# Kernel optimization log

Measured on AMD Instinct MI355X. Metric: run time of the kernel, lower is better.

The kernel has to match this reference:

```python
import jax, jax.numpy as jnp
from jax import lax
import numpy as np

EMA_ALPHA = 0.3
LN_EPS = 1e-5
SW = 5  # center_window_size


def _gelu(x):
    return jax.nn.gelu(x, approximate=False)  # torch nn.GELU default = exact erf


def _layernorm(x, g, b):
    mu = x.mean(-1, keepdims=True)
    var = ((x - mu) ** 2).mean(-1, keepdims=True)
    return (x - mu) * lax.rsqrt(var + LN_EPS) * g + b


def _ema_scan(x, alpha):
    # x: [B, T, C]; x_smooth[t] = lerp(x_smooth[t-1], x[t], alpha)
    x0 = x[:, 0]
    def step(prev, xt):
        s = prev + alpha * (xt - prev)
        return s, s
    _, ys = lax.scan(step, x0, jnp.swapaxes(x[:, 1:], 0, 1))  # [T-1, B, C]
    return jnp.concatenate([x0[:, None], jnp.swapaxes(ys, 0, 1)], axis=1)


def _lstm_dir(x, w_ih, w_hh, b):
    # x: [B, T, Cin]; w_ih: [Cin, 4H]; w_hh: [H, 4H]; b: [4H]. torch gate order i,f,g,o
    B = x.shape[0]
    H = w_hh.shape[0]
    pre = jnp.einsum('btc,ch->bth', x, w_ih) + b  # [B, T, 4H]
    def step(carry, p):
        h, c = carry
        gates = p + h @ w_hh
        i, f, g, o = jnp.split(gates, 4, axis=-1)
        c = jax.nn.sigmoid(f) * c + jax.nn.sigmoid(i) * jnp.tanh(g)
        h = jax.nn.sigmoid(o) * jnp.tanh(c)
        return (h, c), h
    init = (jnp.zeros((B, H), x.dtype), jnp.zeros((B, H), x.dtype))
    _, hs = lax.scan(step, init, jnp.swapaxes(pre, 0, 1))  # [T, B, H]
    return jnp.swapaxes(hs, 0, 1)


def _bilstm(x, wih_f, whh_f, b_f, wih_r, whh_r, b_r):
    fwd = _lstm_dir(x, wih_f, whh_f, b_f)
    bwd = jnp.flip(_lstm_dir(jnp.flip(x, axis=1), wih_r, whh_r, b_r), axis=1)
    return jnp.concatenate([fwd, bwd], axis=-1)  # [B, T, 2H]


def setup_inputs() -> dict:
    key = jax.random.key(0)
    ks = jax.random.split(key, 24)
    B, T, C, BD, O, H = 4096, 31, 768, 128, 12, 64
    AUG = 3 * BD  # 384
    def n(k, shape, s):
        return jax.random.normal(k, shape, dtype=jnp.float32) * s
    return {
        'x': n(ks[0], (B, T, C), 1.0),
        'cls_w': n(ks[1], (C, BD), 0.03), 'cls_b': jnp.zeros((BD,), jnp.float32),
        'delta_w': n(ks[2], (C, BD), 0.03), 'delta_b': jnp.zeros((BD,), jnp.float32),
        'acc_w': n(ks[3], (C, BD), 0.03), 'acc_b': jnp.zeros((BD,), jnp.float32),
        'cls_ln_g': jnp.ones((BD,), jnp.float32), 'cls_ln_b': jnp.zeros((BD,), jnp.float32),
        'delta_ln_g': jnp.ones((BD,), jnp.float32), 'delta_ln_b': jnp.zeros((BD,), jnp.float32),
        'acc_ln_g': jnp.ones((BD,), jnp.float32), 'acc_ln_b': jnp.zeros((BD,), jnp.float32),
        'lin0_w': n(ks[4], (AUG, 256), 0.05), 'lin0_b': jnp.zeros((256,), jnp.float32),
        'gate': jnp.float32(0.2),
        'attn_w': n(ks[5], (2 * H, 1), 0.08), 'attn_b': jnp.zeros((1,), jnp.float32),
        'attn_temp': jnp.float32(1.0),
        'lin1_w': n(ks[6], (C, O), 0.03), 'lin1_b': jnp.zeros((O,), jnp.float32),
        'lin2_w': n(ks[7], (2 * H, O), 0.08), 'lin2_b': jnp.zeros((O,), jnp.float32),
        'lstm_wih_f': n(ks[8], (256, 4 * H), 0.06), 'lstm_whh_f': n(ks[9], (H, 4 * H), 0.12),
        'lstm_b_f': jnp.zeros((4 * H,), jnp.float32),
        'lstm_wih_r': n(ks[10], (256, 4 * H), 0.06), 'lstm_whh_r': n(ks[11], (H, 4 * H), 0.12),
        'lstm_b_r': jnp.zeros((4 * H,), jnp.float32),
    }


def reference(x, cls_w, cls_b, delta_w, delta_b, acc_w, acc_b,
              cls_ln_g, cls_ln_b, delta_ln_g, delta_ln_b, acc_ln_g, acc_ln_b,
              lin0_w, lin0_b, gate, attn_w, attn_b, attn_temp,
              lin1_w, lin1_b, lin2_w, lin2_b,
              lstm_wih_f, lstm_whh_f, lstm_b_f, lstm_wih_r, lstm_whh_r, lstm_b_r):
    T = x.shape[1]
    hsl = T // 2
    l, r = max(0, hsl - SW), min(T, hsl + SW + 1)  # center window [10, 21) for T=31

    # --- robust deltas: EMA smoothing + reflect-padded finite differences ---
    x_smooth = _ema_scan(x, EMA_ALPHA)                       # [B, T, C]
    padded = jnp.pad(x_smooth, ((0, 0), (2, 0), (0, 0)), mode='reflect')  # [B, T+2, C]
    dx = padded[:, 1:] - padded[:, :-1]                       # [B, T+1, C]
    ddx = dx[:, 1:] - dx[:, :-1]                              # [B, T, C]
    delta_stream = dx[:, 1:]                                  # [B, T, C]
    acc_stream = ddx                                          # [B, T, C]

    # --- linear branch: mean of lin1 over center window of smoothed stream ---
    linear_logits = (x_smooth[:, l:r] @ lin1_w + lin1_b).mean(axis=1)  # [B, O]

    # --- bottlenecks (eval mode: dropout identity) + LayerNorms ---
    cls_bn = _layernorm(_gelu(x_smooth @ cls_w + cls_b), cls_ln_g, cls_ln_b)
    delta_bn = _layernorm(_gelu(delta_stream @ delta_w + delta_b), delta_ln_g, delta_ln_b)
    acc_bn = _layernorm(_gelu(acc_stream @ acc_w + acc_b), acc_ln_g, acc_ln_b)
    x_aug = jnp.concatenate([cls_bn, delta_bn, acc_bn], axis=-1)  # [B, T, 384]

    x_lstm = _gelu(x_aug @ lin0_w + lin0_b)                   # [B, T, 256]
    x_lstm = x_lstm - x_lstm.mean(axis=1, keepdims=True)      # center over time (fp32)

    # --- BiLSTM + attention pooling over center window ---
    lstm_out = _bilstm(x_lstm, lstm_wih_f, lstm_whh_f, lstm_b_f,
                       lstm_wih_r, lstm_whh_r, lstm_b_r)      # [B, T, 128]
    window = lstm_out[:, l:r]                                 # [B, W, 128]
    temp = jax.nn.softplus(attn_temp) + 0.001
    scores = (window @ attn_w + attn_b)[..., 0] / temp        # [B, W]
    attn = jax.nn.softmax(scores, axis=1)[..., None]          # [B, W, 1]
    attended = (attn * window).sum(axis=1)                    # [B, 128]
    lstm_logits = attended @ lin2_w + lin2_b                  # [B, O]

    g = jax.nn.sigmoid(gate)
    final_logits = linear_logits + g * (lstm_logits - linear_logits)
    return final_logits, attended
```

## Files before the change

### kernel.cpp

```cpp
#include <hip/hip_runtime.h>
#include <cstdint>
#include <cstddef>


typedef short s8v __attribute__((ext_vector_type(8)));
typedef float f4v __attribute__((ext_vector_type(4)));

#if defined(__has_builtin)
#if __has_builtin(__builtin_amdgcn_global_load_lds)
#define HAVE_GLL 1
#endif
#endif
#ifndef HAVE_GLL
#define HAVE_GLL 0
#endif

__device__ __forceinline__ unsigned short f2bf(float f) {
  union { float f; unsigned int u; } v; v.f = f;
  unsigned int u = v.u;
  return (unsigned short)((u + 0x7fffu + ((u >> 16) & 1u)) >> 16);
}
__device__ __forceinline__ float bf2f(unsigned short h) {
  union { unsigned int u; float f; } v; v.u = ((unsigned int)h) << 16;
  return v.f;
}
__device__ __forceinline__ float fsig(float x) {
  return __fdividef(1.f, 1.f + __expf(-x));
}
__device__ __forceinline__ float ftanh(float x) {
  return 1.f - __fdividef(2.f, 1.f + __expf(2.f * x));
}
__device__ __forceinline__ float fgelu(float x) {
  return 0.5f * x * (1.f + erff(x * 0.70710678118654752f));
}

__device__ __forceinline__ void ld_lds16(const unsigned short* g,
                                         unsigned short* ldsU, int lane) {
#if HAVE_GLL
  __builtin_amdgcn_global_load_lds(
      (__attribute__((address_space(1))) void*)(uintptr_t)(const void*)g,
      (__attribute__((address_space(3))) void*)(unsigned int)(uintptr_t)(void*)ldsU,
      16, 0, 0);
#else
  *(uint4*)(ldsU + lane * 8) = *(const uint4*)g;
#endif
}
__device__ __forceinline__ void wait_vm0() {
#if HAVE_GLL
  __builtin_amdgcn_s_waitcnt(0x0F70);
#endif
}

#define OFF_W1T   0u
#define OFF_W2T   589824u
#define OFF_WIHT  786432u
#define OFF_WHHT  1048576u
#define OFF_XS    1114112u
#define OFF_XW    196149248u
#define OFF_LL    208732160u
#define OFF_WIN   208928768u
#define OFF_XAUG  220463104u
#define OFF_XLSTM 317980672u

__global__ __launch_bounds__(256) void k0_prep(
    const float* __restrict__ cls_w, const float* __restrict__ delta_w,
    const float* __restrict__ acc_w, const float* __restrict__ lin0_w,
    const float* __restrict__ wih_f, const float* __restrict__ wih_r,
    const float* __restrict__ whh_f, const float* __restrict__ whh_r,
    unsigned short* __restrict__ ws) {
  int i = blockIdx.x * 256 + threadIdx.x;
  if (i < 294912) {
    int n = i / 768, k = i - n * 768;
    int seg = n >> 7, nn = n & 127;
    const float* w = seg == 0 ? cls_w : (seg == 1 ? delta_w : acc_w);
    ws[i] = f2bf(w[k * 128 + nn]);
  } else if (i < 393216) {
    int j = i - 294912;
    int n = j / 384, k = j - n * 384;
    ws[i] = f2bf(lin0_w[k * 256 + n]);
  } else if (i < 524288) {
    int j = i - 393216;
    int n = j >> 8, k = j & 255;
    ws[i] = f2bf(n < 256 ? wih_f[k * 256 + n] : wih_r[k * 256 + (n - 256)]);
  } else if (i < 557056) {
    int j = i - 524288;
    int d = j >> 14, rem = j & 16383;
    int n = rem >> 6, k = rem & 63;
    const float* w = d ? whh_r : whh_f;
    ws[i] = f2bf(w[k * 256 + n]);
  }
}

__global__ __launch_bounds__(256) void k1_ema(
    const float* __restrict__ x, unsigned short* __restrict__ xs,
    float* __restrict__ xw) {
  int gid = blockIdx.x * 256 + threadIdx.x;
  int b = gid / 768;
  int c = gid - b * 768;
  size_t base = (size_t)b * 31 * 768 + c;
  float s = x[base];
  xs[base] = f2bf(s);
  float wsum = 0.f;
#pragma unroll
  for (int t = 1; t < 31; ++t) {
    float xv = x[base + t * 768];
    s = s + 0.3f * (xv - s);
    xs[base + t * 768] = f2bf(s);
    if (t >= 10 && t <= 20) wsum += s;
  }
  xw[gid] = wsum * (1.f / 11.f);
}

__global__ __launch_bounds__(64) void k1b_linlog(
    const float* __restrict__ xw, const float* __restrict__ lin1_w,
    const float* __restrict__ lin1_b, float* __restrict__ ll) {
  int b = blockIdx.x;
  int lane = threadIdx.x;
  float p[12];
#pragma unroll
  for (int o = 0; o < 12; ++o) p[o] = 0.f;
  for (int k = lane; k < 768; k += 64) {
    float xv = xw[b * 768 + k];
    const float* w = lin1_w + k * 12;
#pragma unroll
    for (int o = 0; o < 12; ++o) p[o] += xv * w[o];
  }
#pragma unroll
  for (int o = 0; o < 12; ++o) {
    float v = p[o];
#pragma unroll
    for (int s = 1; s < 64; s <<= 1) v += __shfl_xor(v, s, 64);
    p[o] = v;
  }
  if (lane == 0) {
#pragma unroll
    for (int o = 0; o < 12; ++o) ll[b * 12 + o] = p[o] + lin1_b[o];
  }
}

template <int KDIM>
__device__ __forceinline__ void gemm128(
    const unsigned short* __restrict__ A, int rowClamp,
    const unsigned short* __restrict__ Bt,
    unsigned short* sA, unsigned short* sB, f4v acc[4][4]) {
  const int tid  = threadIdx.x;
  const int lane = tid & 63;
  const int wv   = tid >> 6;
  const int l15  = lane & 15;
  const int quad = lane >> 4;
  const int mh   = (wv >> 1) * 64;
  const int nh   = (wv & 1) * 64;

  const int srow = wv * 32 + (lane >> 3);
  const int scol = (lane & 7) * 8;
  const unsigned short* aBase[4];
  const unsigned short* bBase[4];
  unsigned short* aDst[4];
  unsigned short* bDst[4];
#pragma unroll
  for (int j = 0; j < 4; ++j) {
    int r = srow + j * 8;
    int ar = r < rowClamp ? r : rowClamp;
    aBase[j] = A + (size_t)ar * KDIM + scol;
    bBase[j] = Bt + (size_t)r * KDIM + scol;
    aDst[j] = sA + (wv * 4 + j) * 512;
    bDst[j] = sB + (wv * 4 + j) * 512;
  }
#pragma unroll
  for (int mt = 0; mt < 4; ++mt)
#pragma unroll
    for (int nt = 0; nt < 4; ++nt)
      acc[mt][nt] = (f4v){0.f, 0.f, 0.f, 0.f};

  constexpr int KT = KDIM / 64;
  for (int kt = 0; kt < KT; ++kt) {
    if (kt) __syncthreads();
    int ko = kt * 64;
#pragma unroll
    for (int j = 0; j < 4; ++j) ld_lds16(aBase[j] + ko, aDst[j], lane);
#pragma unroll
    for (int j = 0; j < 4; ++j) ld_lds16(bBase[j] + ko, bDst[j], lane);
    wait_vm0();
    __syncthreads();
#pragma unroll
    for (int ks = 0; ks < 2; ++ks) {
      s8v af[4], bfv[4];
#pragma unroll
      for (int mt = 0; mt < 4; ++mt)
        af[mt] = *(const s8v*)(&sA[(mh + mt * 16 + l15) * 64 + ks * 32 + quad * 8]);
#pragma unroll
      for (int nt = 0; nt < 4; ++nt)
        bfv[nt] = *(const s8v*)(&sB[(nh + nt * 16 + l15) * 64 + ks * 32 + quad * 8]);
#pragma unroll
      for (int mt = 0; mt < 4; ++mt)
#pragma unroll
        for (int nt = 0; nt < 4; ++nt)
          acc[mt][nt] = __builtin_amdgcn_mfma_f32_16x16x32_bf16(af[mt], bfv[nt], acc[mt][nt], 0, 0, 0);
    }
  }
  __syncthreads();
}

__device__ __forceinline__ void dump_chunk(f4v acc[4][4], float* sP, int lo,
                                           int nrows, int pstr) {
  const int tid  = threadIdx.x;
  const int lane = tid & 63;
  const int wv   = tid >> 6;
  const int l15  = lane & 15;
  const int quad = lane >> 4;
  const int mh   = (wv >> 1) * 64;
  const int nh   = (wv & 1) * 64;
#pragma unroll
  for (int mt = 0; mt < 4; ++mt)
#pragma unroll
    for (int nt = 0; nt < 4; ++nt)
#pragma unroll
      for (int r = 0; r < 4; ++r) {
        int rr = mh + mt * 16 + quad * 4 + r - lo;
        if ((unsigned)rr < (unsigned)nrows)
          sP[rr * pstr + nh + nt * 16 + l15] = acc[mt][nt][r];
      }
}

__device__ __forceinline__ float stencil_gelu3(const float* sP, const float* sBias,
                                               int seg, int t, int c) {
  const float* p = sP + t * 390 + seg * 130 + c;
  float v;
  if (seg == 0) {
    v = p[0];
  } else if (seg == 1) {
    v = (t == 0) ? (p[0] - p[390]) : (p[0] - p[-390]);
  } else {
    if (t == 0)      v = p[0] - 2.f * p[390] + p[780];
    else if (t == 1) v = 2.f * (p[0] - p[-390]);
    else             v = p[0] - 2.f * p[-390] + p[-780];
  }
  return fgelu(v + sBias[seg * 128 + c]);
}

__global__ __launch_bounds__(1024) void k2_aug(
    const unsigned short* __restrict__ xs, const unsigned short* __restrict__ W1t,
    const float* __restrict__ cls_b, const float* __restrict__ delta_b,
    const float* __restrict__ acc_b,
    const float* __restrict__ g0, const float* __restrict__ be0,
    const float* __restrict__ g1, const float* __restrict__ be1,
    const float* __restrict__ g2, const float* __restrict__ be2,
    unsigned short* __restrict__ xaug) {
  __shared__ __align__(16) char smem[131072];
  unsigned short* buf0 = (unsigned short*)smem;
  unsigned short* buf1 = (unsigned short*)(smem + 65536);
  float* sP    = (float*)smem;
  float* sBias = (float*)(smem + 65536);
  float* sG    = sBias + 384;
  float* sLb   = sG + 384;
  float* sMu   = sLb + 384;
  float* sRs   = sMu + 93;

  const int tid  = threadIdx.x;
  const int lane = tid & 63;
  const int wv   = tid >> 6;
  const int l15  = lane & 15;
  const int quad = lane >> 4;
  const int wm   = wv >> 3;
  const int wn   = wv & 7;
  const int rowBase = blockIdx.x * 124;

  const int subrow = lane >> 3;
  const int schunk = ((lane & 7) ^ subrow) * 8;
  const unsigned short* src[4];
#pragma unroll
  for (int j = 0; j < 4; ++j) {
    int slice = wv * 4 + j;
    int row = slice * 8 + subrow;
    src[j] = (row < 128)
        ? xs + (size_t)(rowBase + (row < 124 ? row : 123)) * 768 + schunk
        : W1t + (size_t)(row - 128) * 768 + schunk;
  }

  f4v acc[4][3];
#pragma unroll
  for (int mt = 0; mt < 4; ++mt)
#pragma unroll
    for (int nt = 0; nt < 3; ++nt) acc[mt][nt] = (f4v){0.f, 0.f, 0.f, 0.f};

  const int swz = (l15 & 7) << 3;

#pragma unroll
  for (int j = 0; j < 4; ++j) ld_lds16(src[j], buf0 + (wv * 4 + j) * 512, lane);
  wait_vm0();
  __syncthreads();

  for (int kt = 0; kt < 12; ++kt) {
    unsigned short* bc = (kt & 1) ? buf1 : buf0;
    unsigned short* bn = (kt & 1) ? buf0 : buf1;
    if (kt < 11) {
#pragma unroll
      for (int j = 0; j < 4; ++j)
        ld_lds16(src[j] + (kt + 1) * 64, bn + (wv * 4 + j) * 512, lane);
    }
#pragma unroll
    for (int ks = 0; ks < 2; ++ks) {
      s8v af[4], bfv[3];
      const int ko = (ks * 32 + quad * 8) ^ swz;
#pragma unroll
      for (int mt = 0; mt < 4; ++mt)
        af[mt] = *(const s8v*)(&bc[(wm * 64 + mt * 16 + l15) * 64 + ko]);
#pragma unroll
      for (int nt = 0; nt < 3; ++nt)
        bfv[nt] = *(const s8v*)(&bc[(128 + wn * 48 + nt * 16 + l15) * 64 + ko]);
#pragma unroll
      for (int mt = 0; mt < 4; ++mt)
#pragma unroll
        for (int nt = 0; nt < 3; ++nt)
          acc[mt][nt] = __builtin_amdgcn_mfma_f32_16x16x32_bf16(af[mt], bfv[nt], acc[mt][nt], 0, 0, 0);
    }
    wait_vm0();
    __syncthreads();
  }

  if (tid < 384) {
    int seg = tid >> 7, c = tid & 127;
    sBias[tid] = seg == 0 ? cls_b[c] : (seg == 1 ? delta_b[c] : acc_b[c]);
    sG[tid]    = seg == 0 ? g0[c]    : (seg == 1 ? g1[c]    : g2[c]);
    sLb[tid]   = seg == 0 ? be0[c]   : (seg == 1 ? be1[c]   : be2[c]);
  }

#pragma unroll
  for (int ck = 0; ck < 4; ++ck) {
    int lo = ck * 31;
#pragma unroll
    for (int mt = 0; mt < 4; ++mt) {
      int rbase = wm * 64 + mt * 16 + quad * 4 - lo;
#pragma unroll
      for (int nt = 0; nt < 3; ++nt) {
        int gcol = wn * 48 + nt * 16;
        int colp = (gcol >> 7) * 130 + (gcol & 127) + l15;
#pragma unroll
        for (int r = 0; r < 4; ++r) {
          int rr = rbase + r;
          if ((unsigned)rr < 31u) sP[rr * 390 + colp] = acc[mt][nt][r];
        }
      }
    }
    __syncthreads();
    if (tid < 744) {
      int seg = tid < 248 ? 0 : (tid < 496 ? 1 : 2);
      int rem = tid - seg * 248;
      int row = rem >> 3, q = rem & 7;
      float sum = 0.f, ss = 0.f;
#pragma unroll
      for (int i = 0; i < 16; ++i) {
        float v = stencil_gelu3(sP, sBias, seg, row, q + 8 * i);
        sum += v; ss += v * v;
      }
      sum += __shfl_xor(sum, 1, 64); ss += __shfl_xor(ss, 1, 64);
      sum += __shfl_xor(sum, 2, 64); ss += __shfl_xor(ss, 2, 64);
      sum += __shfl_xor(sum, 4, 64); ss += __shfl_xor(ss, 4, 64);
      if (q == 0) {
        float mu = sum * (1.f / 128.f);
        sMu[seg * 31 + row] = mu;
        sRs[seg * 31 + row] = rsqrtf(ss * (1.f / 128.f) - mu * mu + 1e-5f);
      }
    }
    __syncthreads();
#pragma unroll
    for (int seg = 0; seg < 3; ++seg) {
      for (int idx = tid; idx < 31 * 128; idx += 1024) {
        int row = idx >> 7, c = idx & 127;
        float v = stencil_gelu3(sP, sBias, seg, row, c);
        float o = (v - sMu[seg * 31 + row]) * sRs[seg * 31 + row]
                  * sG[seg * 128 + c] + sLb[seg * 128 + c];
        xaug[(size_t)(rowBase + lo + row) * 384 + seg * 128 + c] = f2bf(o);
      }
    }
    __syncthreads();
  }
}

__global__ __launch_bounds__(256) void k3_lstm_in(
    const unsigned short* __restrict__ xaug, const unsigned short* __restrict__ W2t,
    const float* __restrict__ lin0_b, unsigned short* __restrict__ xlstm) {
  __shared__ __align__(16) char smem[33792];
  unsigned short* sA = (unsigned short*)smem;
  unsigned short* sB = (unsigned short*)(smem + 16384);
  float* sP  = (float*)smem;
  float* sCM = (float*)(smem + 32768);
  int by = blockIdx.y;
  int rowBase = blockIdx.x * 124;
  f4v acc[4][4];
  gemm128<384>(xaug + (size_t)rowBase * 384, 123, W2t + (size_t)by * 128 * 384, sA, sB, acc);
  int tid = threadIdx.x;
#pragma unroll
  for (int ck = 0; ck < 2; ++ck) {
    int lo = ck * 62;
    dump_chunk(acc, sP, lo, 62, 132);
    __syncthreads();
    for (int idx = tid; idx < 62 * 128; idx += 256) {
      int row = idx >> 7, col = idx & 127;
      sP[row * 132 + col] = fgelu(sP[row * 132 + col] + lin0_b[by * 128 + col]);
    }
    __syncthreads();
    {
      int bb = tid >> 7, col = tid & 127;
      float s = 0.f;
      for (int tr = 0; tr < 31; ++tr) s += sP[(bb * 31 + tr) * 132 + col];
      sCM[tid] = s * (1.f / 31.f);
    }
    __syncthreads();
    for (int idx = tid; idx < 62 * 128; idx += 256) {
      int row = idx >> 7, col = idx & 127;
      int bb = row >= 31 ? 1 : 0;
      float v = sP[row * 132 + col] - sCM[bb * 128 + col];
      xlstm[(size_t)(rowBase + lo + row) * 256 + by * 128 + col] = f2bf(v);
    }
    __syncthreads();
  }
}

__global__ __launch_bounds__(256) void k3b_pre(
    const unsigned short* __restrict__ xlstm, const unsigned short* __restrict__ Wiht,
    const float* __restrict__ b_f, const float* __restrict__ b_r,
    unsigned short* __restrict__ pre) {
  __shared__ __align__(16) char smem[32768];
  unsigned short* sA = (unsigned short*)smem;
  unsigned short* sB = (unsigned short*)(smem + 16384);
  float* sP = (float*)smem;
  int by = blockIdx.y;
  int rowBase = blockIdx.x * 128;
  f4v acc[4][4];
  gemm128<256>(xlstm + (size_t)rowBase * 256, 127, Wiht + (size_t)by * 128 * 256, sA, sB, acc);
  int tid = threadIdx.x;
#pragma unroll
  for (int ck = 0; ck < 2; ++ck) {
    int lo = ck * 64;
    dump_chunk(acc, sP, lo, 64, 128);
    __syncthreads();
    for (int idx = tid; idx < 64 * 128; idx += 256) {
      int row = idx >> 7, col = idx & 127;
      int gcol = by * 128 + col;
      float bias = gcol < 256 ? b_f[gcol] : b_r[gcol - 256];
      pre[(size_t)(rowBase + lo + row) * 512 + gcol] = f2bf(sP[row * 128 + col] + bias);
    }
    __syncthreads();
  }
}

__global__ __launch_bounds__(256) void k4_lstm(
    const unsigned short* __restrict__ pre, const unsigned short* __restrict__ Whht,
    unsigned short* __restrict__ win) {
  __shared__ unsigned short sW[256 * 72];
  __shared__ unsigned short sH[16 * 72];
  __shared__ float sG[16 * 260];
  int tid = threadIdx.x;
  int dir = blockIdx.y;
  int b0  = blockIdx.x * 16;
  {
    const unsigned short* src = Whht + dir * 16384;
#pragma unroll
    for (int c = 0; c < 8; ++c) {
      int id = tid + c * 256;
      int row = id >> 3, kc = (id & 7) * 8;
      uint4 v = *(const uint4*)(src + row * 64 + kc);
      *(uint4*)(&sW[row * 72 + kc]) = v;
    }
  }
  for (int i = tid; i < 16 * 72; i += 256) sH[i] = 0;
  __syncthreads();

  const int lane = tid & 63, wv = tid >> 6, l15 = lane & 15, quad = lane >> 4;
  const int eb = tid >> 4, jb = (tid & 15) * 4;
  float cs[4] = {0.f, 0.f, 0.f, 0.f};

  int tt0 = dir ? 30 : 0;
  const unsigned short* pbase = pre + ((size_t)(b0 + eb) * 31) * 512 + dir * 256;
  ushort4 pi = *(const ushort4*)(pbase + tt0 * 512 + jb);
  ushort4 pf = *(const ushort4*)(pbase + tt0 * 512 + 64 + jb);
  ushort4 pg = *(const ushort4*)(pbase + tt0 * 512 + 128 + jb);
  ushort4 po = *(const ushort4*)(pbase + tt0 * 512 + 192 + jb);

  for (int t = 0; t < 31; ++t) {
    f4v acc[4];
#pragma unroll
    for (int nt = 0; nt < 4; ++nt) acc[nt] = (f4v){0.f, 0.f, 0.f, 0.f};
#pragma unroll
    for (int ks = 0; ks < 2; ++ks) {
      s8v af = *(const s8v*)(&sH[l15 * 72 + ks * 32 + quad * 8]);
#pragma unroll
      for (int nt = 0; nt < 4; ++nt) {
        int n = wv * 64 + nt * 16 + l15;
        s8v bfv = *(const s8v*)(&sW[n * 72 + ks * 32 + quad * 8]);
        acc[nt] = __builtin_amdgcn_mfma_f32_16x16x32_bf16(af, bfv, acc[nt], 0, 0, 0);
      }
    }
#pragma unroll
    for (int nt = 0; nt < 4; ++nt)
#pragma unroll
      for (int r = 0; r < 4; ++r)
        sG[(quad * 4 + r) * 260 + wv * 64 + nt * 16 + l15] = acc[nt][r];

    ushort4 ni, nf, ng, no;
    if (t < 30) {
      int ttn = dir ? 29 - t : t + 1;
      ni = *(const ushort4*)(pbase + ttn * 512 + jb);
      nf = *(const ushort4*)(pbase + ttn * 512 + 64 + jb);
      ng = *(const ushort4*)(pbase + ttn * 512 + 128 + jb);
      no = *(const ushort4*)(pbase + ttn * 512 + 192 + jb);
    }
    __syncthreads();

    int tt = dir ? 30 - t : t;
    const float* g = &sG[eb * 260];
    float hv[4];
#pragma unroll
    for (int jj = 0; jj < 4; ++jj) {
      int j = jb + jj;
      float vi = g[j]       + bf2f(jj == 0 ? pi.x : jj == 1 ? pi.y : jj == 2 ? pi.z : pi.w);
      float vf = g[64 + j]  + bf2f(jj == 0 ? pf.x : jj == 1 ? pf.y : jj == 2 ? pf.z : pf.w);
      float vg = g[128 + j] + bf2f(jj == 0 ? pg.x : jj == 1 ? pg.y : jj == 2 ? pg.z : pg.w);
      float vo = g[192 + j] + bf2f(jj == 0 ? po.x : jj == 1 ? po.y : jj == 2 ? po.z : po.w);
      float cc = fsig(vf) * cs[jj] + fsig(vi) * ftanh(vg);
      cs[jj] = cc;
      hv[jj] = fsig(vo) * ftanh(cc);
    }
    ushort4 hb;
    hb.x = f2bf(hv[0]); hb.y = f2bf(hv[1]); hb.z = f2bf(hv[2]); hb.w = f2bf(hv[3]);
    *(ushort4*)(&sH[eb * 72 + jb]) = hb;
    if (tt >= 10 && tt <= 20)
      *(ushort4*)(win + ((size_t)(b0 + eb) * 11 + (tt - 10)) * 128 + dir * 64 + jb) = hb;
    if (t < 30) { pi = ni; pf = nf; pg = ng; po = no; }
    __syncthreads();
  }
}

__global__ __launch_bounds__(256) void k5_attn(
    const unsigned short* __restrict__ win, const float* __restrict__ attn_w,
    const float* __restrict__ attn_b, const float* __restrict__ attn_t,
    const float* __restrict__ lin2_w, const float* __restrict__ lin2_b,
    const float* __restrict__ linlog, const float* __restrict__ gate,
    float* __restrict__ out) {
  __shared__ unsigned short sWin[176 * 128];
  __shared__ float sAw[128];
  __shared__ float sSc[176];
  __shared__ float sAtt[16 * 128];
  int tid = threadIdx.x;
  int b0  = blockIdx.x * 16;
#pragma unroll
  for (int c = 0; c < 11; ++c) {
    int id = tid + c * 256;
    int row = id >> 4, kc = (id & 15) * 8;
    uint4 v = *(const uint4*)(win + ((size_t)b0 * 11 + row) * 128 + kc);
    *(uint4*)(&sWin[row * 128 + kc]) = v;
  }
  if (tid < 128) sAw[tid] = attn_w[tid];
  __syncthreads();
  if (tid < 176) {
    int b = tid / 11, wt = tid - b * 11;
    const unsigned short* w = &sWin[(b * 11 + wt) * 128];
    float dot = 0.f;
    for (int ch = 0; ch < 128; ++ch) dot += bf2f(w[ch]) * sAw[ch];
    float temp = logf(1.f + __expf(attn_t[0])) + 0.001f;
    sSc[tid] = (dot + attn_b[0]) / temp;
  }
  __syncthreads();
  if (tid < 16) {
    float m = -1e30f;
    for (int wt = 0; wt < 11; ++wt) m = fmaxf(m, sSc[tid * 11 + wt]);
    float e[11], sum = 0.f;
    for (int wt = 0; wt < 11; ++wt) { e[wt] = __expf(sSc[tid * 11 + wt] - m); sum += e[wt]; }
    float inv = __fdividef(1.f, sum);
    for (int wt = 0; wt < 11; ++wt) sSc[tid * 11 + wt] = e[wt] * inv;
  }
  __syncthreads();
#pragma unroll
  for (int p = 0; p < 8; ++p) {
    int task = tid + p * 256;
    int b = task >> 7, ch = task & 127;
    float a = 0.f;
    for (int wt = 0; wt < 11; ++wt)
      a += sSc[b * 11 + wt] * bf2f(sWin[(b * 11 + wt) * 128 + ch]);
    sAtt[b * 128 + ch] = a;
    out[49152 + (size_t)(b0 + b) * 128 + ch] = a;
  }
  __syncthreads();
  if (tid < 192) {
    int b = tid / 12, o = tid - b * 12;
    float dot = 0.f;
    for (int ch = 0; ch < 128; ++ch) dot += sAtt[b * 128 + ch] * lin2_w[ch * 12 + o];
    dot += lin2_b[o];
    float lin = linlog[(size_t)(b0 + b) * 12 + o];
    float gg = fsig(gate[0]);
    out[(size_t)(b0 + b) * 12 + o] = lin + gg * (dot - lin);
  }
}

extern "C" void kernel_launch(void* const* d_in, const int* in_sizes, int n_in,
                              void* d_out, int out_size, void* d_ws, size_t ws_size,
                              hipStream_t stream) {
  const float* x       = (const float*)d_in[0];
  const float* cls_w   = (const float*)d_in[1];
  const float* cls_b   = (const float*)d_in[2];
  const float* delta_w = (const float*)d_in[3];
  const float* delta_b = (const float*)d_in[4];
  const float* acc_w   = (const float*)d_in[5];
  const float* acc_b   = (const float*)d_in[6];
  const float* cls_g   = (const float*)d_in[7];
  const float* cls_be  = (const float*)d_in[8];
  const float* del_g   = (const float*)d_in[9];
  const float* del_be  = (const float*)d_in[10];
  const float* accg    = (const float*)d_in[11];
  const float* accbe   = (const float*)d_in[12];
  const float* lin0_w  = (const float*)d_in[13];
  const float* lin0_b  = (const float*)d_in[14];
  const float* gate    = (const float*)d_in[15];
  const float* attn_w  = (const float*)d_in[16];
  const float* attn_b  = (const float*)d_in[17];
  const float* attn_t  = (const float*)d_in[18];
  const float* lin1_w  = (const float*)d_in[19];
  const float* lin1_b  = (const float*)d_in[20];
  const float* lin2_w  = (const float*)d_in[21];
  const float* lin2_b  = (const float*)d_in[22];
  const float* wih_f   = (const float*)d_in[23];
  const float* whh_f   = (const float*)d_in[24];
  const float* b_f     = (const float*)d_in[25];
  const float* wih_r   = (const float*)d_in[26];
  const float* whh_r   = (const float*)d_in[27];
  const float* b_r     = (const float*)d_in[28];

  char* ws = (char*)d_ws;
  unsigned short* W1t   = (unsigned short*)(ws + OFF_W1T);
  unsigned short* W2t   = (unsigned short*)(ws + OFF_W2T);
  unsigned short* Wiht  = (unsigned short*)(ws + OFF_WIHT);
  unsigned short* Whht  = (unsigned short*)(ws + OFF_WHHT);
  unsigned short* XS    = (unsigned short*)(ws + OFF_XS);
  unsigned short* PRE   = XS;
  float*          XW    = (float*)(ws + OFF_XW);
  float*          LL    = (float*)(ws + OFF_LL);
  unsigned short* WIN   = (unsigned short*)(ws + OFF_WIN);
  unsigned short* XAUG  = (unsigned short*)(ws + OFF_XAUG);
  unsigned short* XLSTM = (unsigned short*)(ws + OFF_XLSTM);
  float* out = (float*)d_out;

  k0_prep<<<2176, 256, 0, stream>>>(cls_w, delta_w, acc_w, lin0_w, wih_f, wih_r,
                                    whh_f, whh_r, (unsigned short*)ws);
  k1_ema<<<12288, 256, 0, stream>>>(x, XS, XW);
  k1b_linlog<<<4096, 64, 0, stream>>>(XW, lin1_w, lin1_b, LL);
  k2_aug<<<1024, 1024, 0, stream>>>(XS, W1t, cls_b, delta_b, acc_b,
                                    cls_g, cls_be, del_g, del_be, accg, accbe, XAUG);
  k3_lstm_in<<<dim3(1024, 2), 256, 0, stream>>>(XAUG, W2t, lin0_b, XLSTM);
  k3b_pre<<<dim3(992, 4), 256, 0, stream>>>(XLSTM, Wiht, b_f, b_r, PRE);
  k4_lstm<<<dim3(256, 2), 256, 0, stream>>>(PRE, Whht, WIN);
  k5_attn<<<256, 256, 0, stream>>>(WIN, attn_w, attn_b, attn_t, lin2_w, lin2_b,
                                   LL, gate, out);
}
```

Before: 1.101 ms.

## Fuse augment, LSTM-input and gate-preactivation GEMMs into one kernel

Merges k2_aug, k3_lstm_in and k3b_pre into a single 512-thread kernel that keeps the 124-row x_aug and x_lstm tiles in LDS. Weight tiles are streamed through double-buffered staging, and only the final gate preactivations go to global memory. This removes the global round trips for the bf16 XAUG and XLSTM intermediates and two kernel launches. In exchange it uses about 152 KB of LDS per block, so each CU holds fewer blocks and there is less latency hiding. The bias, centering and layernorm epilogues are also reorganised with wider per-thread work.

```diff
diff --git a/kernel.cpp b/kernel.cpp
--- a/kernel.cpp
+++ b/kernel.cpp
@@ -59,8 +59,7 @@
 #define OFF_XW    196149248u
 #define OFF_LL    208732160u
 #define OFF_WIN   208928768u
-#define OFF_XAUG  220463104u
-#define OFF_XLSTM 317980672u
+#define OFF_PRE   220463104u
 
 __global__ __launch_bounds__(256) void k0_prep(
     const float* __restrict__ cls_w, const float* __restrict__ delta_w,
@@ -138,185 +137,58 @@
   }
 }
 
-template <int KDIM>
-__device__ __forceinline__ void gemm128(
-    const unsigned short* __restrict__ A, int rowClamp,
-    const unsigned short* __restrict__ Bt,
-    unsigned short* sA, unsigned short* sB, f4v acc[4][4]) {
+__device__ __forceinline__ float stencil_gelu3(const float* sP, const float* sBias,
+                                               int seg, int t, int c) {
+  const float* p = sP + t * 388 + seg * 130 + c;
+  float v;
+  if (seg == 0) {
+    v = p[0];
+  } else if (seg == 1) {
+    v = (t == 0) ? (p[0] - p[388]) : (p[0] - p[-388]);
+  } else {
+    if (t == 0)      v = p[0] - 2.f * p[388] + p[776];
+    else if (t == 1) v = 2.f * (p[0] - p[-388]);
+    else             v = p[0] - 2.f * p[-388] + p[-776];
+  }
+  return fgelu(v + sBias[seg * 128 + c]);
+}
+
+__global__ __launch_bounds__(512, 2) void k2_mega(
+    const unsigned short* __restrict__ xs, const unsigned short* __restrict__ W1t,
+    const unsigned short* __restrict__ W2t, const unsigned short* __restrict__ Wiht,
+    const float* __restrict__ cls_b, const float* __restrict__ delta_b,
+    const float* __restrict__ acc_b,
+    const float* __restrict__ g0, const float* __restrict__ be0,
+    const float* __restrict__ g1, const float* __restrict__ be1,
+    const float* __restrict__ g2, const float* __restrict__ be2,
+    const float* __restrict__ lin0_b, const float* __restrict__ b_f,
+    const float* __restrict__ b_r, unsigned short* __restrict__ pre) {
+  __shared__ __align__(16) char smem[156160];
+  unsigned short* stg1  = (unsigned short*)smem;
+  unsigned short* xaug  = (unsigned short*)smem;
+  unsigned short* xlstm = (unsigned short*)smem;
+  unsigned short* stg3  = (unsigned short*)(smem + 65536);
+  unsigned short* sPb   = (unsigned short*)(smem + 65536);
+  float*          sP1   = (float*)(smem + 98304);
+  unsigned short* stg2  = (unsigned short*)(smem + 98304);
+  float*          sP2   = (float*)(smem + 98304);
+  float* sBias = (float*)(smem + 146688);
+  float* sG    = sBias + 384;
+  float* sLb   = sG + 384;
+  float* sMu   = sLb + 384;
+  float* sRs   = sMu + 93;
+  float* sL0b  = sRs + 93;
+  float* sB3   = sL0b + 256;
+  float* sCM   = sB3 + 512;
+
   const int tid  = threadIdx.x;
   const int lane = tid & 63;
   const int wv   = tid >> 6;
   const int l15  = lane & 15;
   const int quad = lane >> 4;
-  const int mh   = (wv >> 1) * 64;
-  const int nh   = (wv & 1) * 64;
-
-  const int srow = wv * 32 + (lane >> 3);
-  const int scol = (lane & 7) * 8;
-  const unsigned short* aBase[4];
-  const unsigned short* bBase[4];
-  unsigned short* aDst[4];
-  unsigned short* bDst[4];
-#pragma unroll
-  for (int j = 0; j < 4; ++j) {
-    int r = srow + j * 8;
-    int ar = r < rowClamp ? r : rowClamp;
-    aBase[j] = A + (size_t)ar * KDIM + scol;
-    bBase[j] = Bt + (size_t)r * KDIM + scol;
-    aDst[j] = sA + (wv * 4 + j) * 512;
-    bDst[j] = sB + (wv * 4 + j) * 512;
-  }
-#pragma unroll
-  for (int mt = 0; mt < 4; ++mt)
-#pragma unroll
-    for (int nt = 0; nt < 4; ++nt)
-      acc[mt][nt] = (f4v){0.f, 0.f, 0.f, 0.f};
-
-  constexpr int KT = KDIM / 64;
-  for (int kt = 0; kt < KT; ++kt) {
-    if (kt) __syncthreads();
-    int ko = kt * 64;
-#pragma unroll
-    for (int j = 0; j < 4; ++j) ld_lds16(aBase[j] + ko, aDst[j], lane);
-#pragma unroll
-    for (int j = 0; j < 4; ++j) ld_lds16(bBase[j] + ko, bDst[j], lane);
-    wait_vm0();
-    __syncthreads();
-#pragma unroll
-    for (int ks = 0; ks < 2; ++ks) {
-      s8v af[4], bfv[4];
-#pragma unroll
-      for (int mt = 0; mt < 4; ++mt)
-        af[mt] = *(const s8v*)(&sA[(mh + mt * 16 + l15) * 64 + ks * 32 + quad * 8]);
-#pragma unroll
-      for (int nt = 0; nt < 4; ++nt)
-        bfv[nt] = *(const s8v*)(&sB[(nh + nt * 16 + l15) * 64 + ks * 32 + quad * 8]);
-#pragma unroll
-      for (int mt = 0; mt < 4; ++mt)
-#pragma unroll
-        for (int nt = 0; nt < 4; ++nt)
-          acc[mt][nt] = __builtin_amdgcn_mfma_f32_16x16x32_bf16(af[mt], bfv[nt], acc[mt][nt], 0, 0, 0);
-    }
-  }
-  __syncthreads();
-}
-
-__device__ __forceinline__ void dump_chunk(f4v acc[4][4], float* sP, int lo,
-                                           int nrows, int pstr) {
-  const int tid  = threadIdx.x;
-  const int lane = tid & 63;
-  const int wv   = tid >> 6;
-  const int l15  = lane & 15;
-  const int quad = lane >> 4;
-  const int mh   = (wv >> 1) * 64;
-  const int nh   = (wv & 1) * 64;
-#pragma unroll
-  for (int mt = 0; mt < 4; ++mt)
-#pragma unroll
-    for (int nt = 0; nt < 4; ++nt)
-#pragma unroll
-      for (int r = 0; r < 4; ++r) {
-        int rr = mh + mt * 16 + quad * 4 + r - lo;
-        if ((unsigned)rr < (unsigned)nrows)
-          sP[rr * pstr + nh + nt * 16 + l15] = acc[mt][nt][r];
-      }
-}
-
-__device__ __forceinline__ float stencil_gelu3(const float* sP, const float* sBias,
-                                               int seg, int t, int c) {
-  const float* p = sP + t * 390 + seg * 130 + c;
-  float v;
-  if (seg == 0) {
-    v = p[0];
-  } else if (seg == 1) {
-    v = (t == 0) ? (p[0] - p[390]) : (p[0] - p[-390]);
-  } else {
-    if (t == 0)      v = p[0] - 2.f * p[390] + p[780];
-    else if (t == 1) v = 2.f * (p[0] - p[-390]);
-    else             v = p[0] - 2.f * p[-390] + p[-780];
-  }
-  return fgelu(v + sBias[seg * 128 + c]);
-}
-
-__global__ __launch_bounds__(1024) void k2_aug(
-    const unsigned short* __restrict__ xs, const unsigned short* __restrict__ W1t,
-    const float* __restrict__ cls_b, const float* __restrict__ delta_b,
-    const float* __restrict__ acc_b,
-    const float* __restrict__ g0, const float* __restrict__ be0,
-    const float* __restrict__ g1, const float* __restrict__ be1,
-    const float* __restrict__ g2, const float* __restrict__ be2,
-    unsigned short* __restrict__ xaug) {
-  __shared__ __align__(16) char smem[131072];
-  unsigned short* buf0 = (unsigned short*)smem;
-  unsigned short* buf1 = (unsigned short*)(smem + 65536);
-  float* sP    = (float*)smem;
-  float* sBias = (float*)(smem + 65536);
-  float* sG    = sBias + 384;
-  float* sLb   = sG + 384;
-  float* sMu   = sLb + 384;
-  float* sRs   = sMu + 93;
-
-  const int tid  = threadIdx.x;
-  const int lane = tid & 63;
-  const int wv   = tid >> 6;
-  const int l15  = lane & 15;
-  const int quad = lane >> 4;
-  const int wm   = wv >> 3;
-  const int wn   = wv & 7;
+  const int wm   = wv >> 2;
+  const int wn   = wv & 3;
   const int rowBase = blockIdx.x * 124;
-
-  const int subrow = lane >> 3;
-  const int schunk = ((lane & 7) ^ subrow) * 8;
-  const unsigned short* src[4];
-#pragma unroll
-  for (int j = 0; j < 4; ++j) {
-    int slice = wv * 4 + j;
-    int row = slice * 8 + subrow;
-    src[j] = (row < 128)
-        ? xs + (size_t)(rowBase + (row < 124 ? row : 123)) * 768 + schunk
-        : W1t + (size_t)(row - 128) * 768 + schunk;
-  }
-
-  f4v acc[4][3];
-#pragma unroll
-  for (int mt = 0; mt < 4; ++mt)
-#pragma unroll
-    for (int nt = 0; nt < 3; ++nt) acc[mt][nt] = (f4v){0.f, 0.f, 0.f, 0.f};
-
-  const int swz = (l15 & 7) << 3;
-
-#pragma unroll
-  for (int j = 0; j < 4; ++j) ld_lds16(src[j], buf0 + (wv * 4 + j) * 512, lane);
-  wait_vm0();
-  __syncthreads();
-
-  for (int kt = 0; kt < 12; ++kt) {
-    unsigned short* bc = (kt & 1) ? buf1 : buf0;
-    unsigned short* bn = (kt & 1) ? buf0 : buf1;
-    if (kt < 11) {
-#pragma unroll
-      for (int j = 0; j < 4; ++j)
-        ld_lds16(src[j] + (kt + 1) * 64, bn + (wv * 4 + j) * 512, lane);
-    }
-#pragma unroll
-    for (int ks = 0; ks < 2; ++ks) {
-      s8v af[4], bfv[3];
-      const int ko = (ks * 32 + quad * 8) ^ swz;
-#pragma unroll
-      for (int mt = 0; mt < 4; ++mt)
-        af[mt] = *(const s8v*)(&bc[(wm * 64 + mt * 16 + l15) * 64 + ko]);
-#pragma unroll
-      for (int nt = 0; nt < 3; ++nt)
-        bfv[nt] = *(const s8v*)(&bc[(128 + wn * 48 + nt * 16 + l15) * 64 + ko]);
-#pragma unroll
-      for (int mt = 0; mt < 4; ++mt)
-#pragma unroll
-        for (int nt = 0; nt < 3; ++nt)
-          acc[mt][nt] = __builtin_amdgcn_mfma_f32_16x16x32_bf16(af[mt], bfv[nt], acc[mt][nt], 0, 0, 0);
-    }
-    wait_vm0();
-    __syncthreads();
-  }
 
   if (tid < 384) {
     int seg = tid >> 7, c = tid & 127;
@@ -324,38 +196,89 @@
     sG[tid]    = seg == 0 ? g0[c]    : (seg == 1 ? g1[c]    : g2[c]);
     sLb[tid]   = seg == 0 ? be0[c]   : (seg == 1 ? be1[c]   : be2[c]);
   }
-
-#pragma unroll
+  if (tid < 256) sL0b[tid] = lin0_b[tid];
+  sB3[tid] = tid < 256 ? b_f[tid] : b_r[tid - 256];
+
+  const int subrow  = lane >> 3;
+  const int schunk8 = ((lane & 7) ^ subrow) * 8;
+  const int swz     = (l15 & 7) << 3;
+  const unsigned short* src1[8];
+#pragma unroll
+  for (int j = 0; j < 8; ++j) {
+    int row = (wv * 8 + j) * 8 + subrow;
+    src1[j] = (row < 128)
+        ? xs + (size_t)(rowBase + (row < 124 ? row : 123)) * 768 + schunk8
+        : W1t + (size_t)(row - 128) * 768 + schunk8;
+  }
+
+  f4v acc1[4][6];
+#pragma unroll
+  for (int mt = 0; mt < 4; ++mt)
+#pragma unroll
+    for (int nt = 0; nt < 6; ++nt) acc1[mt][nt] = (f4v){0.f, 0.f, 0.f, 0.f};
+
+#pragma unroll
+  for (int j = 0; j < 8; ++j) ld_lds16(src1[j], stg1 + (wv * 8 + j) * 512, lane);
+  wait_vm0();
+  __syncthreads();
+
+  for (int kt = 0; kt < 12; ++kt) {
+    unsigned short* bc = stg1 + (kt & 1) * 32768;
+    unsigned short* bn = stg1 + ((kt & 1) ^ 1) * 32768;
+    if (kt < 11) {
+#pragma unroll
+      for (int j = 0; j < 8; ++j)
+        ld_lds16(src1[j] + (kt + 1) * 64, bn + (wv * 8 + j) * 512, lane);
+    }
+#pragma unroll
+    for (int ks = 0; ks < 2; ++ks) {
+      const int ko = (ks * 32 + quad * 8) ^ swz;
+      s8v af[4], bfv[6];
+#pragma unroll
+      for (int mt = 0; mt < 4; ++mt)
+        af[mt] = *(const s8v*)(&bc[(wm * 64 + mt * 16 + l15) * 64 + ko]);
+#pragma unroll
+      for (int nt = 0; nt < 6; ++nt)
+        bfv[nt] = *(const s8v*)(&bc[(128 + wn * 96 + nt * 16 + l15) * 64 + ko]);
+#pragma unroll
+      for (int mt = 0; mt < 4; ++mt)
+#pragma unroll
+        for (int nt = 0; nt < 6; ++nt)
+          acc1[mt][nt] = __builtin_amdgcn_mfma_f32_16x16x32_bf16(af[mt], bfv[nt], acc1[mt][nt], 0, 0, 0);
+    }
+    wait_vm0();
+    __syncthreads();
+  }
+
   for (int ck = 0; ck < 4; ++ck) {
-    int lo = ck * 31;
+    const int lo = ck * 31;
 #pragma unroll
     for (int mt = 0; mt < 4; ++mt) {
       int rbase = wm * 64 + mt * 16 + quad * 4 - lo;
 #pragma unroll
-      for (int nt = 0; nt < 3; ++nt) {
-        int gcol = wn * 48 + nt * 16;
+      for (int nt = 0; nt < 6; ++nt) {
+        int gcol = wn * 96 + nt * 16;
         int colp = (gcol >> 7) * 130 + (gcol & 127) + l15;
 #pragma unroll
         for (int r = 0; r < 4; ++r) {
           int rr = rbase + r;
-          if ((unsigned)rr < 31u) sP[rr * 390 + colp] = acc[mt][nt][r];
+          if ((unsigned)rr < 31u) sP1[rr * 388 + colp] = acc1[mt][nt][r];
         }
       }
     }
     __syncthreads();
-    if (tid < 744) {
-      int seg = tid < 248 ? 0 : (tid < 496 ? 1 : 2);
-      int rem = tid - seg * 248;
-      int row = rem >> 3, q = rem & 7;
+    if (tid < 372) {
+      int seg = tid < 124 ? 0 : (tid < 248 ? 1 : 2);
+      int rem = tid - seg * 124;
+      int row = rem >> 2, q = rem & 3;
       float sum = 0.f, ss = 0.f;
 #pragma unroll
-      for (int i = 0; i < 16; ++i) {
-        float v = stencil_gelu3(sP, sBias, seg, row, q + 8 * i);
+      for (int i = 0; i < 32; ++i) {
+        float v = stencil_gelu3(sP1, sBias, seg, row, q + 4 * i);
         sum += v; ss += v * v;
       }
       sum += __shfl_xor(sum, 1, 64); ss += __shfl_xor(ss, 1, 64);
       sum += __shfl_xor(sum, 2, 64); ss += __shfl_xor(ss, 2, 64);
-      sum += __shfl_xor(sum, 4, 64); ss += __shfl_xor(ss, 4, 64);
       if (q == 0) {
         float mu = sum * (1.f / 128.f);
         sMu[seg * 31 + row] = mu;
@@ -365,83 +288,164 @@
     __syncthreads();
 #pragma unroll
     for (int seg = 0; seg < 3; ++seg) {
-      for (int idx = tid; idx < 31 * 128; idx += 1024) {
-        int row = idx >> 7, c = idx & 127;
-        float v = stencil_gelu3(sP, sBias, seg, row, c);
-        float o = (v - sMu[seg * 31 + row]) * sRs[seg * 31 + row]
-                  * sG[seg * 128 + c] + sLb[seg * 128 + c];
-        xaug[(size_t)(rowBase + lo + row) * 384 + seg * 128 + c] = f2bf(o);
-      }
-    }
-    __syncthreads();
-  }
-}
-
-__global__ __launch_bounds__(256) void k3_lstm_in(
-    const unsigned short* __restrict__ xaug, const unsigned short* __restrict__ W2t,
-    const float* __restrict__ lin0_b, unsigned short* __restrict__ xlstm) {
-  __shared__ __align__(16) char smem[33792];
-  unsigned short* sA = (unsigned short*)smem;
-  unsigned short* sB = (unsigned short*)(smem + 16384);
-  float* sP  = (float*)smem;
-  float* sCM = (float*)(smem + 32768);
-  int by = blockIdx.y;
-  int rowBase = blockIdx.x * 124;
-  f4v acc[4][4];
-  gemm128<384>(xaug + (size_t)rowBase * 384, 123, W2t + (size_t)by * 128 * 384, sA, sB, acc);
-  int tid = threadIdx.x;
-#pragma unroll
-  for (int ck = 0; ck < 2; ++ck) {
-    int lo = ck * 62;
-    dump_chunk(acc, sP, lo, 62, 132);
-    __syncthreads();
-    for (int idx = tid; idx < 62 * 128; idx += 256) {
-      int row = idx >> 7, col = idx & 127;
-      sP[row * 132 + col] = fgelu(sP[row * 132 + col] + lin0_b[by * 128 + col]);
-    }
-    __syncthreads();
-    {
-      int bb = tid >> 7, col = tid & 127;
+      for (int idx = tid; idx < 31 * 64; idx += 512) {
+        int row = idx >> 6, cp = (idx & 63) * 2;
+        float v0 = stencil_gelu3(sP1, sBias, seg, row, cp);
+        float v1 = stencil_gelu3(sP1, sBias, seg, row, cp + 1);
+        float mu = sMu[seg * 31 + row], rs = sRs[seg * 31 + row];
+        float o0 = (v0 - mu) * rs * sG[seg * 128 + cp]     + sLb[seg * 128 + cp];
+        float o1 = (v1 - mu) * rs * sG[seg * 128 + cp + 1] + sLb[seg * 128 + cp + 1];
+        unsigned int u = (unsigned int)f2bf(o0) | ((unsigned int)f2bf(o1) << 16);
+        *(unsigned int*)(&xaug[(size_t)(lo + row) * 392 + seg * 128 + cp]) = u;
+      }
+    }
+    __syncthreads();
+  }
+
+  f4v acc2[4][4];
+#pragma unroll
+  for (int mt = 0; mt < 4; ++mt)
+#pragma unroll
+    for (int nt = 0; nt < 4; ++nt) acc2[mt][nt] = (f4v){0.f, 0.f, 0.f, 0.f};
+  {
+    const int r2 = lane >> 2;
+    const int c2 = ((lane & 3) ^ (r2 & 3)) * 8;
+    const unsigned short* src2[2];
+#pragma unroll
+    for (int j = 0; j < 2; ++j)
+      src2[j] = W2t + (size_t)((wv * 2 + j) * 16 + r2) * 384 + c2;
+#pragma unroll
+    for (int j = 0; j < 2; ++j) ld_lds16(src2[j], stg2 + (wv * 2 + j) * 512, lane);
+    wait_vm0();
+    __syncthreads();
+    const int bko = (quad ^ (l15 & 3)) << 3;
+    for (int kt = 0; kt < 12; ++kt) {
+      unsigned short* bc = stg2 + (kt & 1) * 8192;
+      unsigned short* bn = stg2 + ((kt & 1) ^ 1) * 8192;
+      if (kt < 11) {
+#pragma unroll
+        for (int j = 0; j < 2; ++j)
+          ld_lds16(src2[j] + (kt + 1) * 32, bn + (wv * 2 + j) * 512, lane);
+      }
+      s8v af[4], bfv[4];
+#pragma unroll
+      for (int mt = 0; mt < 4; ++mt)
+        af[mt] = *(const s8v*)(&xaug[(size_t)(wm * 64 + mt * 16 + l15) * 392 + kt * 32 + quad * 8]);
+#pragma unroll
+      for (int nt = 0; nt < 4; ++nt)
+        bfv[nt] = *(const s8v*)(&bc[(wn * 64 + nt * 16 + l15) * 32 + bko]);
+#pragma unroll
+      for (int mt = 0; mt < 4; ++mt)
+#pragma unroll
+        for (int nt = 0; nt < 4; ++nt)
+          acc2[mt][nt] = __builtin_amdgcn_mfma_f32_16x16x32_bf16(af[mt], bfv[nt], acc2[mt][nt], 0, 0, 0);
+      wait_vm0();
+      __syncthreads();
+    }
+  }
+
+  for (int ck = 0; ck < 4; ++ck) {
+    const int lo = ck * 31;
+#pragma unroll
+    for (int mt = 0; mt < 4; ++mt) {
+      int rbase = wm * 64 + mt * 16 + quad * 4 - lo;
+#pragma unroll
+      for (int nt = 0; nt < 4; ++nt) {
+        int col = wn * 64 + nt * 16 + l15;
+#pragma unroll
+        for (int r = 0; r < 4; ++r) {
+          int rr = rbase + r;
+          if ((unsigned)rr < 31u) sP2[rr * 260 + col] = acc2[mt][nt][r];
+        }
+      }
+    }
+    __syncthreads();
+    for (int idx = tid; idx < 31 * 256; idx += 512) {
+      int row = idx >> 8, col = idx & 255;
+      sP2[row * 260 + col] = fgelu(sP2[row * 260 + col] + sL0b[col]);
+    }
+    __syncthreads();
+    if (tid < 256) {
       float s = 0.f;
-      for (int tr = 0; tr < 31; ++tr) s += sP[(bb * 31 + tr) * 132 + col];
+      for (int tr = 0; tr < 31; ++tr) s += sP2[tr * 260 + tid];
       sCM[tid] = s * (1.f / 31.f);
     }
     __syncthreads();
-    for (int idx = tid; idx < 62 * 128; idx += 256) {
-      int row = idx >> 7, col = idx & 127;
-      int bb = row >= 31 ? 1 : 0;
-      float v = sP[row * 132 + col] - sCM[bb * 128 + col];
-      xlstm[(size_t)(rowBase + lo + row) * 256 + by * 128 + col] = f2bf(v);
-    }
-    __syncthreads();
-  }
-}
-
-__global__ __launch_bounds__(256) void k3b_pre(
-    const unsigned short* __restrict__ xlstm, const unsigned short* __restrict__ Wiht,
-    const float* __restrict__ b_f, const float* __restrict__ b_r,
-    unsigned short* __restrict__ pre) {
-  __shared__ __align__(16) char smem[32768];
-  unsigned short* sA = (unsigned short*)smem;
-  unsigned short* sB = (unsigned short*)(smem + 16384);
-  float* sP = (float*)smem;
-  int by = blockIdx.y;
-  int rowBase = blockIdx.x * 128;
-  f4v acc[4][4];
-  gemm128<256>(xlstm + (size_t)rowBase * 256, 127, Wiht + (size_t)by * 128 * 256, sA, sB, acc);
-  int tid = threadIdx.x;
-#pragma unroll
-  for (int ck = 0; ck < 2; ++ck) {
-    int lo = ck * 64;
-    dump_chunk(acc, sP, lo, 64, 128);
-    __syncthreads();
-    for (int idx = tid; idx < 64 * 128; idx += 256) {
-      int row = idx >> 7, col = idx & 127;
-      int gcol = by * 128 + col;
-      float bias = gcol < 256 ? b_f[gcol] : b_r[gcol - 256];
-      pre[(size_t)(rowBase + lo + row) * 512 + gcol] = f2bf(sP[row * 128 + col] + bias);
-    }
-    __syncthreads();
+    for (int idx = tid; idx < 31 * 128; idx += 512) {
+      int row = idx >> 7, cp = (idx & 127) * 2;
+      float v0 = sP2[row * 260 + cp]     - sCM[cp];
+      float v1 = sP2[row * 260 + cp + 1] - sCM[cp + 1];
+      unsigned int u = (unsigned int)f2bf(v0) | ((unsigned int)f2bf(v1) << 16);
+      *(unsigned int*)(&xlstm[(size_t)(lo + row) * 260 + cp]) = u;
+    }
+    __syncthreads();
+  }
+
+  f4v acc3[4][4];
+  for (int p = 0; p < 2; ++p) {
+    const unsigned short* src3[4];
+#pragma unroll
+    for (int j = 0; j < 4; ++j)
+      src3[j] = Wiht + (size_t)(p * 256 + (wv * 4 + j) * 8 + subrow) * 256 + schunk8;
+#pragma unroll
+    for (int mt = 0; mt < 4; ++mt)
+#pragma unroll
+      for (int nt = 0; nt < 4; ++nt) acc3[mt][nt] = (f4v){0.f, 0.f, 0.f, 0.f};
+#pragma unroll
+    for (int j = 0; j < 4; ++j) ld_lds16(src3[j], stg3 + (wv * 4 + j) * 512, lane);
+    wait_vm0();
+    __syncthreads();
+    for (int kt = 0; kt < 4; ++kt) {
+      unsigned short* bc = stg3 + (kt & 1) * 16384;
+      unsigned short* bn = stg3 + ((kt & 1) ^ 1) * 16384;
+      if (kt < 3) {
+#pragma unroll
+        for (int j = 0; j < 4; ++j)
+          ld_lds16(src3[j] + (kt + 1) * 64, bn + (wv * 4 + j) * 512, lane);
+      }
+#pragma unroll
+      for (int ks = 0; ks < 2; ++ks) {
+        const int ko = (ks * 32 + quad * 8) ^ swz;
+        s8v af[4], bfv[4];
+#pragma unroll
+        for (int mt = 0; mt < 4; ++mt)
+          af[mt] = *(const s8v*)(&xlstm[(size_t)(wm * 64 + mt * 16 + l15) * 260 + kt * 64 + ks * 32 + quad * 8]);
+#pragma unroll
+        for (int nt = 0; nt < 4; ++nt)
+          bfv[nt] = *(const s8v*)(&bc[(wn * 64 + nt * 16 + l15) * 64 + ko]);
+#pragma unroll
+        for (int mt = 0; mt < 4; ++mt)
+#pragma unroll
+          for (int nt = 0; nt < 4; ++nt)
+            acc3[mt][nt] = __builtin_amdgcn_mfma_f32_16x16x32_bf16(af[mt], bfv[nt], acc3[mt][nt], 0, 0, 0);
+      }
+      wait_vm0();
+      __syncthreads();
+    }
+    for (int ck = 0; ck < 4; ++ck) {
+      const int lo = ck * 31;
+#pragma unroll
+      for (int mt = 0; mt < 4; ++mt) {
+        int rbase = wm * 64 + mt * 16 + quad * 4 - lo;
+#pragma unroll
+        for (int nt = 0; nt < 4; ++nt) {
+          int col = wn * 64 + nt * 16 + l15;
+          float bias = sB3[p * 256 + col];
+#pragma unroll
+          for (int r = 0; r < 4; ++r) {
+            int rr = rbase + r;
+            if ((unsigned)rr < 31u) sPb[rr * 264 + col] = f2bf(acc3[mt][nt][r] + bias);
+          }
+        }
+      }
+      __syncthreads();
+      for (int u = tid; u < 992; u += 512) {
+        int row = u >> 5, cq = (u & 31) * 8;
+        *(uint4*)(pre + (size_t)(rowBase + lo + row) * 512 + p * 256 + cq) =
+            *(const uint4*)(&sPb[row * 264 + cq]);
+      }
+      __syncthreads();
+    }
   }
 }
 
@@ -632,22 +636,19 @@
   unsigned short* Wiht  = (unsigned short*)(ws + OFF_WIHT);
   unsigned short* Whht  = (unsigned short*)(ws + OFF_WHHT);
   unsigned short* XS    = (unsigned short*)(ws + OFF_XS);
-  unsigned short* PRE   = XS;
   float*          XW    = (float*)(ws + OFF_XW);
   float*          LL    = (float*)(ws + OFF_LL);
   unsigned short* WIN   = (unsigned short*)(ws + OFF_WIN);
-  unsigned short* XAUG  = (unsigned short*)(ws + OFF_XAUG);
-  unsigned short* XLSTM = (unsigned short*)(ws + OFF_XLSTM);
+  unsigned short* PRE   = (unsigned short*)(ws + OFF_PRE);
   float* out = (float*)d_out;
 
   k0_prep<<<2176, 256, 0, stream>>>(cls_w, delta_w, acc_w, lin0_w, wih_f, wih_r,
                                     whh_f, whh_r, (unsigned short*)ws);
   k1_ema<<<12288, 256, 0, stream>>>(x, XS, XW);
   k1b_linlog<<<4096, 64, 0, stream>>>(XW, lin1_w, lin1_b, LL);
-  k2_aug<<<1024, 1024, 0, stream>>>(XS, W1t, cls_b, delta_b, acc_b,
-                                    cls_g, cls_be, del_g, del_be, accg, accbe, XAUG);
-  k3_lstm_in<<<dim3(1024, 2), 256, 0, stream>>>(XAUG, W2t, lin0_b, XLSTM);
-  k3b_pre<<<dim3(992, 4), 256, 0, stream>>>(XLSTM, Wiht, b_f, b_r, PRE);
+  k2_mega<<<1024, 512, 0, stream>>>(XS, W1t, W2t, Wiht, cls_b, delta_b, acc_b,
+                                    cls_g, cls_be, del_g, del_be, accg, accbe,
+                                    lin0_b, b_f, b_r, PRE);
   k4_lstm<<<dim3(256, 2), 256, 0, stream>>>(PRE, Whht, WIN);
   k5_attn<<<256, 256, 0, stream>>>(WIN, attn_w, attn_b, attn_t, lin2_w, lin2_b,
                                    LL, gate, out);
```

Result: slower. 1.392 ms (+26.4%).
